# Optimization experiments

Measured on AMD Instinct MI355X. Metric: run time of the kernel, lower is better.

The kernel has to match this reference:

```python
import jax, jax.numpy as jnp
import numpy as np
from jax import lax

B, D, N = 1024, 1024, 65536
M, Ks, DS = 8, 256, 128      # key PQ: subvectors, codewords, subvec dim (D/M)
MV, DV = 8, 256              # value PQ: subvectors, subvec dim (OUT/MV)
OUT = MV * DV
K_TOP = 64


def setup_inputs() -> dict:
    key = jax.random.key(0)
    ks = jax.random.split(key, 7)
    x = jax.random.normal(ks[0], (B, D), dtype=jnp.float32)
    # whitening matrix starts as identity in the module; perturb slightly for a non-trivial test
    whitening_matrix = jnp.eye(D, dtype=jnp.float32) + 0.01 * jax.random.normal(ks[1], (D, D), dtype=jnp.float32)
    key_codebooks = jax.random.normal(ks[2], (M, Ks, DS), dtype=jnp.float32)
    value_codebooks = jax.random.normal(ks[3], (MV, Ks, DV), dtype=jnp.float32)
    bias = jnp.zeros((OUT,), dtype=jnp.float32)
    key_codes = jax.random.randint(ks[4], (N, M), 0, Ks, dtype=jnp.int32)
    value_codes = jax.random.randint(ks[5], (N, MV), 0, Ks, dtype=jnp.int32)
    return {
        "x": x,
        "whitening_matrix": whitening_matrix,
        "key_codebooks": key_codebooks,
        "value_codebooks": value_codebooks,
        "bias": bias,
        "key_codes": key_codes,
        "value_codes": value_codes,
        "k": K_TOP,
    }


def reference(x, whitening_matrix, key_codebooks, value_codebooks, bias, key_codes, value_codes, k):
    # 1) whiten the query (module buffer 'whitening_matrix')
    q = x @ whitening_matrix                      # [B, D]
    qs = q.reshape(B, M, DS)                      # [B, M, DS] query subvectors

    # 2) ADC distance tables: squared L2 between each query subvector and each codeword
    #    dt[b, m, c] = ||qs[b,m] - cb[m,c]||^2
    q_sq = jnp.sum(qs * qs, axis=-1)              # [B, M]
    c_sq = jnp.sum(key_codebooks * key_codebooks, axis=-1)  # [M, Ks]
    cross = jnp.einsum("bmd,mcd->bmc", qs, key_codebooks)   # [B, M, Ks]
    dt = q_sq[:, :, None] + c_sq[None, :, :] - 2.0 * cross  # [B, M, Ks]

    # 3) asymmetric distance to all N stored keys via code gather (irregular access)
    lut = dt.transpose(1, 0, 2)                   # [M, B, Ks]
    # per-subvector gather then sum: d[b, n] = sum_m lut[m, b, key_codes[n, m]]
    dists = jax.vmap(lambda l, c: l[:, c])(lut, key_codes.T).sum(axis=0)  # [B, N]

    # 4) top-k nearest neighbors
    neg_top, top_idx = lax.top_k(-dists, k)       # [B, k]

    # 5) reconstruct values of retrieved neighbors from value PQ codebooks
    vc = value_codes[top_idx]                     # [B, k, MV] int codes
    vals = value_codebooks[jnp.arange(MV)[None, None, :], vc]  # [B, k, MV, DV]
    vals = vals.reshape(vals.shape[0], vals.shape[1], OUT)      # [B, k, OUT]

    # 6) distance-weighted aggregation (softmax over negative distances) + bias
    w = jax.nn.softmax(neg_top, axis=-1)          # [B, k]
    y = jnp.einsum("bk,bko->bo", w, vals) + bias  # [B, OUT]
    return y
```

## Files before the change

kernel.cpp:

```cpp
#include <hip/hip_runtime.h>

#define N_ITEMS 65536

__launch_bounds__(256)
__global__ void gemm_q_kernel(const float* __restrict__ A,
                              const float* __restrict__ W,
                              float* __restrict__ qpart) {
  __shared__ float As[16][132];
  __shared__ float Bs[16][132];
  const int tid = threadIdx.x;
  const int tx = tid & 15, ty = tid >> 4;
  const int rb = blockIdx.y * 128, cb = blockIdx.x * 128;
  const int kz = blockIdx.z * 256;
  const int ar = tid >> 2, ac = (tid & 3) << 2;
  const int bk = tid >> 5, bc = (tid & 31) << 2;

  float4 va0 = *(const float4*)&A[(rb + ar) * 1024 + kz + ac];
  float4 va1 = *(const float4*)&A[(rb + ar + 64) * 1024 + kz + ac];
  float4 vb0 = *(const float4*)&W[(kz + bk) * 1024 + cb + bc];
  float4 vb1 = *(const float4*)&W[(kz + bk + 8) * 1024 + cb + bc];

  float acc[8][8] = {};
  for (int k0 = 0; k0 < 256; k0 += 16) {
    As[ac + 0][ar] = va0.x; As[ac + 1][ar] = va0.y;
    As[ac + 2][ar] = va0.z; As[ac + 3][ar] = va0.w;
    As[ac + 0][ar + 64] = va1.x; As[ac + 1][ar + 64] = va1.y;
    As[ac + 2][ar + 64] = va1.z; As[ac + 3][ar + 64] = va1.w;
    *(float4*)&Bs[bk][bc] = vb0;
    *(float4*)&Bs[bk + 8][bc] = vb1;
    __syncthreads();
    if (k0 + 16 < 256) {
      va0 = *(const float4*)&A[(rb + ar) * 1024 + kz + k0 + 16 + ac];
      va1 = *(const float4*)&A[(rb + ar + 64) * 1024 + kz + k0 + 16 + ac];
      vb0 = *(const float4*)&W[(kz + k0 + 16 + bk) * 1024 + cb + bc];
      vb1 = *(const float4*)&W[(kz + k0 + 16 + bk + 8) * 1024 + cb + bc];
    }
#pragma unroll
    for (int kk = 0; kk < 16; kk++) {
      const float4 a0 = *(const float4*)&As[kk][ty << 2];
      const float4 a1 = *(const float4*)&As[kk][64 + (ty << 2)];
      const float4 b0 = *(const float4*)&Bs[kk][tx << 2];
      const float4 b1 = *(const float4*)&Bs[kk][64 + (tx << 2)];
      const float ar8[8] = {a0.x, a0.y, a0.z, a0.w, a1.x, a1.y, a1.z, a1.w};
      const float br8[8] = {b0.x, b0.y, b0.z, b0.w, b1.x, b1.y, b1.z, b1.w};
#pragma unroll
      for (int r = 0; r < 8; r++)
#pragma unroll
        for (int c = 0; c < 8; c++)
          acc[r][c] = fmaf(ar8[r], br8[c], acc[r][c]);
    }
    __syncthreads();
  }
  float* outp = qpart + blockIdx.z * 1048576;
#pragma unroll
  for (int rh = 0; rh < 2; rh++)
#pragma unroll
    for (int r = 0; r < 4; r++) {
      const int row = rb + rh * 64 + (ty << 2) + r;
      const int ri = rh * 4 + r;
      *(float4*)&outp[row * 1024 + cb + (tx << 2)] =
          make_float4(acc[ri][0], acc[ri][1], acc[ri][2], acc[ri][3]);
      *(float4*)&outp[row * 1024 + cb + 64 + (tx << 2)] =
          make_float4(acc[ri][4], acc[ri][5], acc[ri][6], acc[ri][7]);
    }
}

__launch_bounds__(256)
__global__ void lut_kernel(const float* __restrict__ qpart,
                           const float* __restrict__ kcb,
                           const int* __restrict__ key_codes,
                           float* __restrict__ lut,
                           unsigned long long* __restrict__ pcodes,
                           uint4* __restrict__ poffs) {
  if (blockIdx.z == 8) {
    const int g0 = (((int)blockIdx.y * 4 + (int)blockIdx.x) * 256 + (int)threadIdx.x) * 4;
#pragma unroll
    for (int t = 0; t < 4; t++) {
      const int gid = g0 + t;
      unsigned long long p = 0ull;
      unsigned h[8];
#pragma unroll
      for (int j = 0; j < 8; j++) {
        const unsigned c = (unsigned)key_codes[gid * 8 + j] & 255u;
        p |= (unsigned long long)c << (8 * j);
        h[j] = ((c >> 1) << 7) | ((c & 1u) << 3);
      }
      pcodes[gid] = p;
      poffs[gid] = make_uint4(h[0] | (h[1] << 16), h[2] | (h[3] << 16),
                              h[4] | (h[5] << 16), h[6] | (h[7] << 16));
    }
    return;
  }

  __shared__ float As[32][68];
  __shared__ float Bs[32][68];
  const int tid = threadIdx.x;
  const int tx = tid & 15, ty = tid >> 4;
  const int m = blockIdx.z;
  const int rb = blockIdx.y * 64;
  const int cb0 = blockIdx.x * 64;
  float acc[4][4] = {};
  float qa[4] = {}, cs[4] = {};
  for (int k0 = 0; k0 < 128; k0 += 32) {
#pragma unroll
    for (int l = 0; l < 2; l++) {
      const int e = tid + l * 256;
      const int row = e >> 3, c4 = (e & 7) << 2;
      const int qidx = (rb + row) * 1024 + m * 128 + k0 + c4;
      const float4 p0 = *(const float4*)&qpart[qidx];
      const float4 p1 = *(const float4*)&qpart[qidx + 1048576];
      const float4 p2 = *(const float4*)&qpart[qidx + 2097152];
      const float4 p3 = *(const float4*)&qpart[qidx + 3145728];
      const float4 va = make_float4(p0.x + p1.x + p2.x + p3.x,
                                    p0.y + p1.y + p2.y + p3.y,
                                    p0.z + p1.z + p2.z + p3.z,
                                    p0.w + p1.w + p2.w + p3.w);
      As[c4 + 0][row] = va.x; As[c4 + 1][row] = va.y;
      As[c4 + 2][row] = va.z; As[c4 + 3][row] = va.w;
      const float4 vb = *(const float4*)&kcb[(m * 256 + cb0 + row) * 128 + k0 + c4];
      Bs[c4 + 0][row] = vb.x; Bs[c4 + 1][row] = vb.y;
      Bs[c4 + 2][row] = vb.z; Bs[c4 + 3][row] = vb.w;
    }
    __syncthreads();
#pragma unroll
    for (int kk = 0; kk < 32; kk++) {
      const float4 a = *(const float4*)&As[kk][ty << 2];
      const float4 b = *(const float4*)&Bs[kk][tx << 2];
      const float ar[4] = {a.x, a.y, a.z, a.w};
      const float br[4] = {b.x, b.y, b.z, b.w};
#pragma unroll
      for (int r = 0; r < 4; r++)
#pragma unroll
        for (int c = 0; c < 4; c++)
          acc[r][c] = fmaf(ar[r], br[c], acc[r][c]);
#pragma unroll
      for (int r = 0; r < 4; r++) qa[r] = fmaf(ar[r], ar[r], qa[r]);
#pragma unroll
      for (int c = 0; c < 4; c++) cs[c] = fmaf(br[c], br[c], cs[c]);
    }
    __syncthreads();
  }
#pragma unroll
  for (int r = 0; r < 4; r++) {
    const int row = rb + (ty << 2) + r;
    const int col = cb0 + (tx << 2);
    float4 v;
    v.x = qa[r] + cs[0] - 2.0f * acc[r][0];
    v.y = qa[r] + cs[1] - 2.0f * acc[r][1];
    v.z = qa[r] + cs[2] - 2.0f * acc[r][2];
    v.w = qa[r] + cs[3] - 2.0f * acc[r][3];
    *(float4*)&lut[row * 2048 + m * 256 + col] = v;
  }
}

extern __shared__ char dyn_lds[];

__launch_bounds__(1024)
__global__ void scan4r_kernel(const float* __restrict__ lut,
                              const uint4* __restrict__ poffs,
                              unsigned* __restrict__ cand_d,
                              unsigned short* __restrict__ cand_n) {
  char* repb = dyn_lds;
  short* temps = (short*)(dyn_lds + 131072);
  unsigned long long* tempq = (unsigned long long*)(dyn_lds + 131072);
  const int tid = threadIdx.x;
  const int g = blockIdx.x;

  {
    const int w = tid >> 6, lane = tid & 63;
#pragma unroll
    for (int t0 = 0; t0 < 2; t0++) {
      const int t = w + t0 * 16;
      const int rr = t & 3, seg = t >> 2;
      const int row = (g << 2) + rr;
      const int e0 = seg * 256 + lane * 4;
      const float4 v4 = *(const float4*)&lut[row * 2048 + e0];
      float s4 = v4.x + v4.y + v4.z + v4.w;
#pragma unroll
      for (int off = 32; off > 0; off >>= 1) s4 += __shfl_xor(s4, off);
      const float mean = s4 * (1.0f / 256.0f);
      const float vals[4] = {v4.x, v4.y, v4.z, v4.w};
#pragma unroll
      for (int k = 0; k < 4; k++) {
        float f = (vals[k] - mean) * 64.0f;
        f = fmaxf(fminf(f, 32000.0f), -32000.0f);
        temps[(e0 + k) * 4 + rr] = (short)(int)rintf(f);
      }
    }
  }
  __syncthreads();

  {
    const int lane = tid & 63;
    const unsigned long long q0 = tempq[tid * 2];
    const unsigned long long q1 = tempq[tid * 2 + 1];
    const uint4 wv = make_uint4((unsigned)q0, (unsigned)(q0 >> 32),
                                (unsigned)q1, (unsigned)(q1 >> 32));
    uint4* repv = (uint4*)dyn_lds;
    const int base = tid * 8;
#pragma unroll
    for (int k = 0; k < 8; k++) {
      const int r = (k + lane) & 7;
      repv[base + r] = wv;
    }
  }
  __syncthreads();

  const int r = tid & 7;
  const char* base0 = repb + (r << 4);
  const char* base1 = repb + 65536 + (r << 4);
  unsigned k0[4], k1[4];
#pragma unroll
  for (int j = 0; j < 4; j++) { k0[j] = 0xFFFFFFFFu; k1[j] = 0xFFFFFFFFu; }

  uint2 A[8], B[8];

  auto issue = [&](uint2 (&BUF)[8], const uint4 cw) {
    BUF[0] = *(const uint2*)(base0 + (cw.x & 0xFFFFu));
    BUF[1] = *(const uint2*)(base0 + (cw.x >> 16) + 16384);
    BUF[2] = *(const uint2*)(base0 + (cw.y & 0xFFFFu) + 32768);
    BUF[3] = *(const uint2*)(base0 + (cw.y >> 16) + 49152);
    BUF[4] = *(const uint2*)(base1 + (cw.z & 0xFFFFu));
    BUF[5] = *(const uint2*)(base1 + (cw.z >> 16) + 16384);
    BUF[6] = *(const uint2*)(base1 + (cw.w & 0xFFFFu) + 32768);
    BUF[7] = *(const uint2*)(base1 + (cw.w >> 16) + 49152);
  };

  auto consume = [&](const uint2 (&BUF)[8], const int it) {
    int s0, s1, s2, s3;
    {
      const unsigned lo = BUF[0].x, hi = BUF[0].y;
      s0 = (int)(short)lo; s1 = ((int)lo) >> 16;
      s2 = (int)(short)hi; s3 = ((int)hi) >> 16;
    }
#pragma unroll
    for (int j = 1; j < 8; j++) {
      const unsigned lo = BUF[j].x, hi = BUF[j].y;
      s0 += (int)(short)lo; s1 += ((int)lo) >> 16;
      s2 += (int)(short)hi; s3 += ((int)hi) >> 16;
    }
    const int ss[4] = {s0, s1, s2, s3};
#pragma unroll
    for (int j = 0; j < 4; j++) {
      const unsigned key = ((unsigned)(ss[j] + 0x40000) << 6) | (unsigned)it;
      const unsigned mx = (k0[j] > key) ? k0[j] : key;
      k0[j] = (k0[j] < key) ? k0[j] : key;
      k1[j] = (k1[j] < mx) ? k1[j] : mx;
    }
  };

  {
    const uint4 cA = poffs[tid];
    issue(A, cA);
  }
  uint4 cNxt = poffs[tid + 1024];

  for (int it = 0; it < 64; it += 2) {
    const uint4 c2 = poffs[tid + (((it + 2) & 63) << 10)];
    const uint4 c3 = poffs[tid + (((it + 3) & 63) << 10)];
    issue(B, cNxt);
    consume(A, it);
    issue(A, c2);
    consume(B, it + 1);
    cNxt = c3;
  }

#pragma unroll
  for (int j = 0; j < 4; j++) {
    const int row = (g << 2) + j;
    const int d0 = (int)(k0[j] >> 6) - 0x40000;
    const int d1 = (int)(k1[j] >> 6) - 0x40000;
    const int n0 = tid + (int)((k0[j] & 63u) << 10);
    const int n1 = tid + (int)((k1[j] & 63u) << 10);
    const int ba = row * 2048 + tid * 2;
    *(uint2*)&cand_d[ba] = make_uint2((unsigned)(d0 + 0x40000000),
                                      (unsigned)(d1 + 0x40000000));
    *(unsigned*)&cand_n[ba] = (unsigned)n0 | ((unsigned)n1 << 16);
  }
}

__launch_bounds__(512)
__global__ void scan16_kernel(const float* __restrict__ lut,
                              const unsigned long long* __restrict__ pcodes,
                              unsigned* __restrict__ cand_d,
                              unsigned short* __restrict__ cand_n) {
  __shared__ short sRep[32768];
  const int tid = threadIdx.x;
  const int b = blockIdx.x;

  const float4 v4 = *(const float4*)&lut[b * 2048 + tid * 4];
  float s4 = v4.x + v4.y + v4.z + v4.w;
#pragma unroll
  for (int off = 32; off > 0; off >>= 1) s4 += __shfl_xor(s4, off);
  const float mean = s4 * (1.0f / 256.0f);

  const float vals[4] = {v4.x, v4.y, v4.z, v4.w};
#pragma unroll
  for (int k2 = 0; k2 < 4; k2++) {
    float f = (vals[k2] - mean) * 64.0f;
    f = fmaxf(fminf(f, 32000.0f), -32000.0f);
    const int iv = (int)rintf(f);
    const unsigned hw = (unsigned)(unsigned short)iv;
    const unsigned wrd = hw | (hw << 16);
    const uint4 wv = make_uint4(wrd, wrd, wrd, wrd);
    const int e = tid * 4 + k2;
    *(uint4*)&((unsigned*)sRep)[e * 8] = wv;
    *(uint4*)&((unsigned*)sRep)[e * 8 + 4] = wv;
  }
  __syncthreads();

  const int r = tid & 15;
  int d0 = 0x7FFFFFFF, d1 = 0x7FFFFFFF, d2 = 0x7FFFFFFF, d3 = 0x7FFFFFFF;
  int i0 = 0, i1 = 0, i2 = 0, i3 = 0;

  unsigned long long c8 = pcodes[tid];
  for (int it = 0; it < 128; it++) {
    const int n = tid + (it << 9);
    unsigned long long nxt = 0ull;
    if (it < 127) nxt = pcodes[n + 512];
    const unsigned lo = (unsigned)c8;
    const unsigned hi = (unsigned)(c8 >> 32);
    int s;
    s  = sRep[(((lo      ) & 255u) << 4) + r        ];
    s += sRep[(((lo >>  8) & 255u) << 4) + r +  4096];
    s += sRep[(((lo >> 16) & 255u) << 4) + r +  8192];
    s += sRep[(((lo >> 24)       ) << 4) + r + 12288];
    s += sRep[(((hi      ) & 255u) << 4) + r + 16384];
    s += sRep[(((hi >>  8) & 255u) << 4) + r + 20480];
    s += sRep[(((hi >> 16) & 255u) << 4) + r + 24576];
    s += sRep[(((hi >> 24)       ) << 4) + r + 28672];
    if (s < d3) {
      if (s < d1) {
        if (s < d0) { d3 = d2; i3 = i2; d2 = d1; i2 = i1; d1 = d0; i1 = i0; d0 = s; i0 = n; }
        else        { d3 = d2; i3 = i2; d2 = d1; i2 = i1; d1 = s; i1 = n; }
      } else {
        if (s < d2) { d3 = d2; i3 = i2; d2 = s; i2 = n; }
        else        { d3 = s; i3 = n; }
      }
    }
    c8 = nxt;
  }

  const int base = b * 2048 + tid * 4;
  const uint4 dv = make_uint4((unsigned)(d0 + 0x40000000), (unsigned)(d1 + 0x40000000),
                              (unsigned)(d2 + 0x40000000), (unsigned)(d3 + 0x40000000));
  *(uint4*)&cand_d[base] = dv;
  const unsigned ni01 = (unsigned)i0 | ((unsigned)i1 << 16);
  const unsigned ni23 = (unsigned)i2 | ((unsigned)i3 << 16);
  *(uint2*)&cand_n[base] = make_uint2(ni01, ni23);
}

__launch_bounds__(256)
__global__ void select_kernel(const unsigned* __restrict__ cand_d,
                              const unsigned short* __restrict__ cand_n,
                              const int* __restrict__ value_codes,
                              const float* __restrict__ vcb,
                              const float* __restrict__ bias,
                              float* __restrict__ out) {
  __shared__ unsigned sredw[4];
  __shared__ unsigned long long clist[256];
  __shared__ float sw[256];
  __shared__ int svc[2048];
  __shared__ int scnt;
  __shared__ float sWsum;

  const int tid = threadIdx.x;
  const int b = blockIdx.x;

  const uint4 a0 = *(const uint4*)&cand_d[b * 2048 + tid * 8];
  const uint4 a1 = *(const uint4*)&cand_d[b * 2048 + tid * 8 + 4];
  const uint4 nn = *(const uint4*)&cand_n[b * 2048 + tid * 8];
  unsigned dk[8] = {a0.x, a0.y, a0.z, a0.w, a1.x, a1.y, a1.z, a1.w};
  unsigned ni[8] = {nn.x & 0xFFFFu, nn.x >> 16, nn.y & 0xFFFFu, nn.y >> 16,
                    nn.z & 0xFFFFu, nn.z >> 16, nn.w & 0xFFFFu, nn.w >> 16};

  if (tid == 0) scnt = 0;
  unsigned mn = dk[0];
#pragma unroll
  for (int j = 1; j < 8; j++) mn = (dk[j] < mn) ? dk[j] : mn;
#pragma unroll
  for (int off = 32; off > 0; off >>= 1) {
    const unsigned o = __shfl_xor(mn, off);
    mn = (o < mn) ? o : mn;
  }
  if ((tid & 63) == 0) sredw[tid >> 6] = mn;
  __syncthreads();
  unsigned sMin = sredw[0];
  sMin = (sredw[1] < sMin) ? sredw[1] : sMin;
  sMin = (sredw[2] < sMin) ? sredw[2] : sMin;
  sMin = (sredw[3] < sMin) ? sredw[3] : sMin;
  const unsigned lim = sMin + 2048u;

  const int lane = tid & 63;
  const unsigned long long lm = (1ull << lane) - 1ull;
#pragma unroll
  for (int j = 0; j < 8; j++) {
    const bool pred = dk[j] <= lim;
    const unsigned long long mask = __ballot(pred);
    int base = 0;
    if (lane == 0 && mask) base = atomicAdd(&scnt, __popcll(mask));
    base = __shfl(base, 0);
    if (pred) {
      const int pos = base + __popcll(mask & lm);
      if (pos < 256) clist[pos] = ((unsigned long long)dk[j] << 32) | ni[j];
    }
  }
  __syncthreads();
  const int cnt = min(scnt, 256);

  if (tid < cnt) {
    const int gap = (int)((unsigned)(clist[tid] >> 32)) - (int)sMin;
    sw[tid] = __expf((float)gap * -0.015625f);
  }
  for (int i = tid; i < (cnt << 3); i += 256)
    svc[i] = value_codes[((int)(clist[i >> 3] & 0xFFFFFFFFu)) * 8 + (i & 7)];
  __syncthreads();

  if (tid < 64) {
    float s = 0.f;
    for (int j = tid; j < cnt; j += 64) s += sw[j];
#pragma unroll
    for (int off = 32; off > 0; off >>= 1) s += __shfl_xor(s, off);
    if (tid == 0) sWsum = s;
  }
  __syncthreads();
  const float inv = 1.0f / sWsum;

  const int c0 = tid << 3;
  const int mv = c0 >> 8;
  const int off = c0 & 255;
  float4 acc0 = make_float4(0.f, 0.f, 0.f, 0.f);
  float4 acc1 = make_float4(0.f, 0.f, 0.f, 0.f);
  const float* vbase = vcb + mv * 65536 + off;
  for (int k = 0; k < cnt; k++) {
    const float w = sw[k];
    const float* vp = vbase + svc[(k << 3) + mv] * 256;
    const float4 v0 = *(const float4*)vp;
    const float4 v1 = *(const float4*)(vp + 4);
    acc0.x = fmaf(w, v0.x, acc0.x); acc0.y = fmaf(w, v0.y, acc0.y);
    acc0.z = fmaf(w, v0.z, acc0.z); acc0.w = fmaf(w, v0.w, acc0.w);
    acc1.x = fmaf(w, v1.x, acc1.x); acc1.y = fmaf(w, v1.y, acc1.y);
    acc1.z = fmaf(w, v1.z, acc1.z); acc1.w = fmaf(w, v1.w, acc1.w);
  }
  const float4 b0 = *(const float4*)&bias[c0];
  const float4 b1 = *(const float4*)&bias[c0 + 4];
  *(float4*)&out[b * 2048 + c0] =
      make_float4(fmaf(acc0.x, inv, b0.x), fmaf(acc0.y, inv, b0.y),
                  fmaf(acc0.z, inv, b0.z), fmaf(acc0.w, inv, b0.w));
  *(float4*)&out[b * 2048 + c0 + 4] =
      make_float4(fmaf(acc1.x, inv, b1.x), fmaf(acc1.y, inv, b1.y),
                  fmaf(acc1.z, inv, b1.z), fmaf(acc1.w, inv, b1.w));
}

extern "C" void kernel_launch(void* const* d_in, const int* in_sizes, int n_in,
                              void* d_out, int out_size, void* d_ws, size_t ws_size,
                              hipStream_t stream) {
  const float* x    = (const float*)d_in[0];
  const float* W    = (const float*)d_in[1];
  const float* kcb  = (const float*)d_in[2];
  const float* vcb  = (const float*)d_in[3];
  const float* bias = (const float*)d_in[4];
  const int* key_codes   = (const int*)d_in[5];
  const int* value_codes = (const int*)d_in[6];
  float* out = (float*)d_out;

  float* qpart = (float*)d_ws;
  float* lut   = qpart + 4194304;
  uint4* poffs = (uint4*)(lut + 2097152);
  unsigned long long* pcodes = (unsigned long long*)(poffs + 65536);
  unsigned* cand_d = (unsigned*)d_ws;
  unsigned short* cand_n = (unsigned short*)(cand_d + 2097152);

  hipLaunchKernelGGL(gemm_q_kernel, dim3(8, 8, 4), dim3(256), 0, stream,
                     x, W, qpart);
  hipLaunchKernelGGL(lut_kernel, dim3(4, 16, 9), dim3(256), 0, stream,
                     qpart, kcb, key_codes, lut, pcodes, poffs);

  const hipError_t attr_rc = hipFuncSetAttribute(
      (const void*)scan4r_kernel, hipFuncAttributeMaxDynamicSharedMemorySize, 147456);
  if (attr_rc == hipSuccess) {
    hipLaunchKernelGGL(scan4r_kernel, dim3(256), dim3(1024), 147456, stream,
                       lut, poffs, cand_d, cand_n);
  } else {
    hipLaunchKernelGGL(scan16_kernel, dim3(1024), dim3(512), 0, stream,
                       lut, pcodes, cand_d, cand_n);
  }

  hipLaunchKernelGGL(select_kernel, dim3(1024), dim3(256), 0, stream,
                     cand_d, cand_n, value_codes, vcb, bias, out);
}
```

Measured before the change: 182.5 us.

## Quantize scan LUT to 8-bit packed sums and rescore candidates exactly in fp32

The candidate scan now quantizes the per-subvector LUT to unsigned 8-bit (unit scale, offset 128) instead of 16-bit at scale 64. Sums are computed as packed SWAR byte-pair adds, and each LDS gather fetches 4 bytes instead of 8. The select kernel recomputes exact fp32 distances for the surviving candidates from pcodes and the float LUT, and uses them for the softmax weights. The 8-bit path uses a tighter candidate window (lim_add=32). This cuts LDS traffic and ALU work in the dominant scan, at the cost of coarser quantization, which raises the risk of missing true top-k neighbors and of clipping at ±127.

```diff
diff --git a/kernel.cpp b/kernel.cpp
--- a/kernel.cpp
+++ b/kernel.cpp
@@ -83,7 +83,7 @@
       for (int j = 0; j < 8; j++) {
         const unsigned c = (unsigned)key_codes[gid * 8 + j] & 255u;
         p |= (unsigned long long)c << (8 * j);
-        h[j] = ((c >> 1) << 7) | ((c & 1u) << 3);
+        h[j] = c << 6;
       }
       pcodes[gid] = p;
       poffs[gid] = make_uint4(h[0] | (h[1] << 16), h[2] | (h[3] << 16),
@@ -156,13 +156,13 @@
 extern __shared__ char dyn_lds[];
 
 __launch_bounds__(1024)
-__global__ void scan4r_kernel(const float* __restrict__ lut,
+__global__ void scan1b_kernel(const float* __restrict__ lut,
                               const uint4* __restrict__ poffs,
                               unsigned* __restrict__ cand_d,
                               unsigned short* __restrict__ cand_n) {
   char* repb = dyn_lds;
-  short* temps = (short*)(dyn_lds + 131072);
-  unsigned long long* tempq = (unsigned long long*)(dyn_lds + 131072);
+  unsigned char* temps = (unsigned char*)(dyn_lds + 131072);
+  unsigned* tempw = (unsigned*)(dyn_lds + 131072);
   const int tid = threadIdx.x;
   const int g = blockIdx.x;
 
@@ -182,9 +182,9 @@
       const float vals[4] = {v4.x, v4.y, v4.z, v4.w};
 #pragma unroll
       for (int k = 0; k < 4; k++) {
-        float f = (vals[k] - mean) * 64.0f;
-        f = fmaxf(fminf(f, 32000.0f), -32000.0f);
-        temps[(e0 + k) * 4 + rr] = (short)(int)rintf(f);
+        int iv = (int)rintf(vals[k] - mean);
+        iv = max(-127, min(127, iv));
+        temps[(e0 + k) * 4 + rr] = (unsigned char)(iv + 128);
       }
     }
   }
@@ -192,57 +192,54 @@
 
   {
     const int lane = tid & 63;
-    const unsigned long long q0 = tempq[tid * 2];
-    const unsigned long long q1 = tempq[tid * 2 + 1];
-    const uint4 wv = make_uint4((unsigned)q0, (unsigned)(q0 >> 32),
-                                (unsigned)q1, (unsigned)(q1 >> 32));
+    const unsigned v0 = tempw[tid * 2];
+    const unsigned v1 = tempw[tid * 2 + 1];
+    const uint4 q0 = make_uint4(v0, v0, v0, v0);
+    const uint4 q1 = make_uint4(v1, v1, v1, v1);
     uint4* repv = (uint4*)dyn_lds;
-    const int base = tid * 8;
-#pragma unroll
-    for (int k = 0; k < 8; k++) {
-      const int r = (k + lane) & 7;
-      repv[base + r] = wv;
-    }
-  }
-  __syncthreads();
-
-  const int r = tid & 7;
-  const char* base0 = repb + (r << 4);
-  const char* base1 = repb + 65536 + (r << 4);
+#pragma unroll
+    for (int k = 0; k < 4; k++) {
+      const int kk = (k + lane) & 3;
+      repv[tid * 8 + kk] = q0;
+      repv[tid * 8 + 4 + kk] = q1;
+    }
+  }
+  __syncthreads();
+
+  const int r = tid & 15;
+  const char* base0 = repb + (r << 2);
+  const char* base1 = repb + 65536 + (r << 2);
   unsigned k0[4], k1[4];
 #pragma unroll
   for (int j = 0; j < 4; j++) { k0[j] = 0xFFFFFFFFu; k1[j] = 0xFFFFFFFFu; }
 
-  uint2 A[8], B[8];
-
-  auto issue = [&](uint2 (&BUF)[8], const uint4 cw) {
-    BUF[0] = *(const uint2*)(base0 + (cw.x & 0xFFFFu));
-    BUF[1] = *(const uint2*)(base0 + (cw.x >> 16) + 16384);
-    BUF[2] = *(const uint2*)(base0 + (cw.y & 0xFFFFu) + 32768);
-    BUF[3] = *(const uint2*)(base0 + (cw.y >> 16) + 49152);
-    BUF[4] = *(const uint2*)(base1 + (cw.z & 0xFFFFu));
-    BUF[5] = *(const uint2*)(base1 + (cw.z >> 16) + 16384);
-    BUF[6] = *(const uint2*)(base1 + (cw.w & 0xFFFFu) + 32768);
-    BUF[7] = *(const uint2*)(base1 + (cw.w >> 16) + 49152);
+  unsigned A[8], B[8];
+
+  auto issue = [&](unsigned (&BUF)[8], const uint4 cw) {
+    BUF[0] = *(const unsigned*)(base0 + (cw.x & 0xFFFFu));
+    BUF[1] = *(const unsigned*)(base0 + (cw.x >> 16) + 16384);
+    BUF[2] = *(const unsigned*)(base0 + (cw.y & 0xFFFFu) + 32768);
+    BUF[3] = *(const unsigned*)(base0 + (cw.y >> 16) + 49152);
+    BUF[4] = *(const unsigned*)(base1 + (cw.z & 0xFFFFu));
+    BUF[5] = *(const unsigned*)(base1 + (cw.z >> 16) + 16384);
+    BUF[6] = *(const unsigned*)(base1 + (cw.w & 0xFFFFu) + 32768);
+    BUF[7] = *(const unsigned*)(base1 + (cw.w >> 16) + 49152);
   };
 
-  auto consume = [&](const uint2 (&BUF)[8], const int it) {
-    int s0, s1, s2, s3;
-    {
-      const unsigned lo = BUF[0].x, hi = BUF[0].y;
-      s0 = (int)(short)lo; s1 = ((int)lo) >> 16;
-      s2 = (int)(short)hi; s3 = ((int)hi) >> 16;
-    }
+  auto consume = [&](const unsigned (&BUF)[8], const int it) {
+    const unsigned M = 0x00FF00FFu;
+    unsigned accA = BUF[0] & M;
+    unsigned accB = (BUF[0] >> 8) & M;
 #pragma unroll
     for (int j = 1; j < 8; j++) {
-      const unsigned lo = BUF[j].x, hi = BUF[j].y;
-      s0 += (int)(short)lo; s1 += ((int)lo) >> 16;
-      s2 += (int)(short)hi; s3 += ((int)hi) >> 16;
-    }
-    const int ss[4] = {s0, s1, s2, s3};
+      accA += BUF[j] & M;
+      accB += (BUF[j] >> 8) & M;
+    }
+    const int ss[4] = {(int)(accA & 0xFFFFu), (int)(accB & 0xFFFFu),
+                       (int)(accA >> 16), (int)(accB >> 16)};
 #pragma unroll
     for (int j = 0; j < 4; j++) {
-      const unsigned key = ((unsigned)(ss[j] + 0x40000) << 6) | (unsigned)it;
+      const unsigned key = ((unsigned)ss[j] << 6) | (unsigned)it;
       const unsigned mx = (k0[j] > key) ? k0[j] : key;
       k0[j] = (k0[j] < key) ? k0[j] : key;
       k1[j] = (k1[j] < mx) ? k1[j] : mx;
@@ -268,13 +265,12 @@
 #pragma unroll
   for (int j = 0; j < 4; j++) {
     const int row = (g << 2) + j;
-    const int d0 = (int)(k0[j] >> 6) - 0x40000;
-    const int d1 = (int)(k1[j] >> 6) - 0x40000;
+    const unsigned d0 = k0[j] >> 6;
+    const unsigned d1 = k1[j] >> 6;
     const int n0 = tid + (int)((k0[j] & 63u) << 10);
     const int n1 = tid + (int)((k1[j] & 63u) << 10);
     const int ba = row * 2048 + tid * 2;
-    *(uint2*)&cand_d[ba] = make_uint2((unsigned)(d0 + 0x40000000),
-                                      (unsigned)(d1 + 0x40000000));
+    *(uint2*)&cand_d[ba] = make_uint2(d0, d1);
     *(unsigned*)&cand_n[ba] = (unsigned)n0 | ((unsigned)n1 << 16);
   }
 }
@@ -356,8 +352,12 @@
                               const int* __restrict__ value_codes,
                               const float* __restrict__ vcb,
                               const float* __restrict__ bias,
+                              const unsigned long long* __restrict__ pcodes,
+                              const float* __restrict__ lutf,
+                              const unsigned lim_add,
                               float* __restrict__ out) {
   __shared__ unsigned sredw[4];
+  __shared__ float sredf[4];
   __shared__ unsigned long long clist[256];
   __shared__ float sw[256];
   __shared__ int svc[2048];
@@ -389,7 +389,7 @@
   sMin = (sredw[1] < sMin) ? sredw[1] : sMin;
   sMin = (sredw[2] < sMin) ? sredw[2] : sMin;
   sMin = (sredw[3] < sMin) ? sredw[3] : sMin;
-  const unsigned lim = sMin + 2048u;
+  const unsigned lim = sMin + lim_add;
 
   const int lane = tid & 63;
   const unsigned long long lm = (1ull << lane) - 1ull;
@@ -408,12 +408,30 @@
   __syncthreads();
   const int cnt = min(scnt, 256);
 
+  float dex = 1e30f;
   if (tid < cnt) {
-    const int gap = (int)((unsigned)(clist[tid] >> 32)) - (int)sMin;
-    sw[tid] = __expf((float)gap * -0.015625f);
+    const int n = (int)(clist[tid] & 0xFFFFFFFFu);
+    const unsigned long long c8 = pcodes[n];
+    const float* lrow = lutf + b * 2048;
+    const unsigned lo = (unsigned)c8, hi = (unsigned)(c8 >> 32);
+    dex  = lrow[        (lo       & 255u)];
+    dex += lrow[ 256 + ((lo >>  8) & 255u)];
+    dex += lrow[ 512 + ((lo >> 16) & 255u)];
+    dex += lrow[ 768 + ((lo >> 24)       )];
+    dex += lrow[1024 + ( hi        & 255u)];
+    dex += lrow[1280 + ((hi >>  8) & 255u)];
+    dex += lrow[1536 + ((hi >> 16) & 255u)];
+    dex += lrow[1792 + ((hi >> 24)       )];
   }
   for (int i = tid; i < (cnt << 3); i += 256)
     svc[i] = value_codes[((int)(clist[i >> 3] & 0xFFFFFFFFu)) * 8 + (i & 7)];
+  float mnf = dex;
+#pragma unroll
+  for (int off = 32; off > 0; off >>= 1) mnf = fminf(mnf, __shfl_xor(mnf, off));
+  if ((tid & 63) == 0) sredf[tid >> 6] = mnf;
+  __syncthreads();
+  const float dminx = fminf(fminf(sredf[0], sredf[1]), fminf(sredf[2], sredf[3]));
+  if (tid < cnt) sw[tid] = __expf(dminx - dex);
   __syncthreads();
 
   if (tid < 64) {
@@ -477,15 +495,19 @@
                      qpart, kcb, key_codes, lut, pcodes, poffs);
 
   const hipError_t attr_rc = hipFuncSetAttribute(
-      (const void*)scan4r_kernel, hipFuncAttributeMaxDynamicSharedMemorySize, 147456);
+      (const void*)scan1b_kernel, hipFuncAttributeMaxDynamicSharedMemorySize, 139264);
+  unsigned lim_add;
   if (attr_rc == hipSuccess) {
-    hipLaunchKernelGGL(scan4r_kernel, dim3(256), dim3(1024), 147456, stream,
+    hipLaunchKernelGGL(scan1b_kernel, dim3(256), dim3(1024), 139264, stream,
                        lut, poffs, cand_d, cand_n);
+    lim_add = 32u;
   } else {
     hipLaunchKernelGGL(scan16_kernel, dim3(1024), dim3(512), 0, stream,
                        lut, pcodes, cand_d, cand_n);
+    lim_add = 2048u;
   }
 
   hipLaunchKernelGGL(select_kernel, dim3(1024), dim3(256), 0, stream,
-                     cand_d, cand_n, value_codes, vcb, bias, out);
+                     cand_d, cand_n, value_codes, vcb, bias, pcodes, lut,
+                     lim_add, out);
 }
```

Measured after the change: 171.2 us. 1.07x faster.
